# Performance work log

Measured on AMD Instinct MI355X. Metric: run time of the kernel, lower is better.

Reference implementation:

```python
import jax, jax.numpy as jnp
import numpy as np

N_NODES = 100000
N_EDGES = 640000
D_IN = 128
D_OUT = 128
D_HID = 128  # assumed MLP hidden width (repo MLP not shown; standard 2-layer GIN MLP)


def setup_inputs() -> dict:
    key = jax.random.key(0)
    k = jax.random.split(key, 8)
    x = jax.random.normal(k[0], (N_NODES, D_IN), dtype=jnp.float32)
    edge_index = jax.random.randint(k[1], (2, N_EDGES), 0, N_NODES, dtype=jnp.int64)
    edge_attr = jax.random.normal(k[2], (N_EDGES, D_IN), dtype=jnp.float32)
    # learned params
    eps = jnp.zeros((), dtype=jnp.float32)  # train_eps=True, init 0
    s1 = 1.0 / np.sqrt(D_IN)
    s2 = 1.0 / np.sqrt(D_HID)
    W1 = jax.random.uniform(k[3], (D_IN, D_HID), jnp.float32, -s1, s1)
    b1 = jax.random.uniform(k[4], (D_HID,), jnp.float32, -s1, s1)
    W2 = jax.random.uniform(k[5], (D_HID, D_OUT), jnp.float32, -s2, s2)
    b2 = jax.random.uniform(k[6], (D_OUT,), jnp.float32, -s2, s2)
    return {"x": x, "edge_index": edge_index, "edge_attr": edge_attr,
            "eps": eps, "W1": W1, "b1": b1, "W2": W2, "b2": b2}


def reference(x, edge_index, edge_attr, eps, W1, b1, W2, b2):
    src = edge_index[0]  # source nodes j
    dst = edge_index[1]  # target nodes i
    # message: ReLU(x_j + edge_attr)  -- [E, D_IN]
    msg = jax.nn.relu(x[src] + edge_attr)
    # scatter-sum aggregation to target nodes -- [N, D_IN]
    aggr = jax.ops.segment_sum(msg, dst, num_segments=N_NODES)
    # GINE update: (1 + eps) * x_i + aggr, then MLP (dropout=0.0 -> identity)
    h = (1.0 + eps) * x + aggr
    h = jax.nn.relu(h @ W1 + b1)
    out = h @ W2 + b2
    return out
```

## Files before the change

kernel.cpp:

```cpp
#include <hip/hip_runtime.h>
#include <hip/hip_bf16.h>

constexpr int NN = 100000;
constexpr int NE = 640000;
constexpr int D  = 128;
constexpr int NB = (NN + 255) / 256;

typedef __attribute__((ext_vector_type(8))) short bf16x8;
typedef __attribute__((ext_vector_type(4))) float f32x4;

__device__ __forceinline__ short f2bf(float f) {
    union { float f; unsigned u; } v; v.f = f;
    unsigned r = v.u + 0x7FFF + ((v.u >> 16) & 1);
    return (short)(r >> 16);
}
__device__ __forceinline__ float bf2f(short h) {
    union { unsigned u; float f; } v;
    v.u = ((unsigned)(unsigned short)h) << 16;
    return v.f;
}
__device__ __forceinline__ unsigned cvtpk(float a, float b) {
    union { __hip_bfloat162 h2; unsigned u; } cv;
    float2 f; f.x = a; f.y = b;
    cv.h2 = __float22bfloat162_rn(f);
    return cv.u;
}
__device__ __forceinline__ void pack_hilo(const float* v, bf16x8& hi, bf16x8& lo) {
#pragma unroll
    for (int i = 0; i < 4; ++i) {
        unsigned u = cvtpk(v[2 * i], v[2 * i + 1]);
        short h0 = (short)(u & 0xFFFF), h1 = (short)(u >> 16);
        hi[2 * i] = h0; hi[2 * i + 1] = h1;
        unsigned ul = cvtpk(v[2 * i] - bf2f(h0), v[2 * i + 1] - bf2f(h1));
        lo[2 * i] = (short)(ul & 0xFFFF); lo[2 * i + 1] = (short)(ul >> 16);
    }
}
__device__ __forceinline__ bf16x8 pack_bf8(const float* v) {
    bf16x8 o;
#pragma unroll
    for (int i = 0; i < 4; ++i) {
        unsigned u = cvtpk(v[2 * i], v[2 * i + 1]);
        o[2 * i] = (short)(u & 0xFFFF); o[2 * i + 1] = (short)(u >> 16);
    }
    return o;
}

__global__ __launch_bounds__(256) void k_zero(int* __restrict__ cnt) {
    int i = blockIdx.x * 256 + threadIdx.x;
    if (i < NN) cnt[i] = 0;
}

__global__ __launch_bounds__(256) void k_hist(const int* __restrict__ dst,
                                              int* __restrict__ cnt) {
    int e = blockIdx.x * 256 + threadIdx.x;
    if (e < NE) atomicAdd(&cnt[dst[e]], 1);
}

__global__ __launch_bounds__(256) void k_bsum(const int* __restrict__ cnt,
                                              int* __restrict__ bsum) {
    int i = blockIdx.x * 256 + threadIdx.x;
    int v = (i < NN) ? cnt[i] : 0;
#pragma unroll
    for (int s = 32; s; s >>= 1) v += __shfl_down(v, s, 64);
    __shared__ int w[4];
    if ((threadIdx.x & 63) == 0) w[threadIdx.x >> 6] = v;
    __syncthreads();
    if (threadIdx.x == 0) bsum[blockIdx.x] = w[0] + w[1] + w[2] + w[3];
}

__global__ __launch_bounds__(512) void k_scan_bsum(const int* __restrict__ bsum,
                                                   int* __restrict__ bboff) {
    int t = threadIdx.x, lane = t & 63;
    int v = (t < NB) ? bsum[t] : 0;
    int incl = v;
#pragma unroll
    for (int s = 1; s < 64; s <<= 1) {
        int u = __shfl_up(incl, s, 64);
        if (lane >= s) incl += u;
    }
    __shared__ int wt[8], wp[8];
    if (lane == 63) wt[t >> 6] = incl;
    __syncthreads();
    if (t == 0) { int run = 0; for (int i = 0; i < 8; ++i) { wp[i] = run; run += wt[i]; } }
    __syncthreads();
    if (t < NB) bboff[t] = incl - v + wp[t >> 6];
}

__global__ __launch_bounds__(256) void k_scan_final(const int* __restrict__ cnt,
                                                    const int* __restrict__ bboff,
                                                    int* __restrict__ off,
                                                    int* __restrict__ cur) {
    int b = blockIdx.x, t = threadIdx.x, lane = t & 63;
    int i = b * 256 + t;
    int v = (i < NN) ? cnt[i] : 0;
    int incl = v;
#pragma unroll
    for (int s = 1; s < 64; s <<= 1) {
        int u = __shfl_up(incl, s, 64);
        if (lane >= s) incl += u;
    }
    __shared__ int wt[4], wp[4];
    if (lane == 63) wt[t >> 6] = incl;
    __syncthreads();
    if (t == 0) { int run = 0; for (int q = 0; q < 4; ++q) { wp[q] = run; run += wt[q]; } }
    __syncthreads();
    int excl = incl - v + wp[t >> 6] + bboff[b];
    if (i < NN) { off[i] = excl; cur[i] = excl; }
    if (i == 0) off[NN] = NE;
}

__global__ __launch_bounds__(256) void k_perm(const int* __restrict__ dst,
                                              const int* __restrict__ src,
                                              int* __restrict__ cur,
                                              int2* __restrict__ ps) {
    int e = blockIdx.x * 256 + threadIdx.x;
    if (e < NE) {
        int p = atomicAdd(&cur[dst[e]], 1);
        int2 v; v.x = e; v.y = src[e];
        ps[p] = v;
    }
}

__global__ __launch_bounds__(256) void k_wsplit(const float* __restrict__ W,
                                                short* __restrict__ Whi,
                                                short* __restrict__ Wlo) {
    for (int idx = blockIdx.x * 256 + threadIdx.x; idx < D * D; idx += gridDim.x * 256) {
        int n = idx >> 7, k = idx & 127;
        float w = W[k * D + n];
        short hi = f2bf(w);
        Whi[idx] = hi;
        Wlo[idx] = f2bf(w - bf2f(hi));
    }
}

constexpr int LDG = 132;

__global__ __launch_bounds__(256) void k_fused(const float* __restrict__ x,
                                               const float* __restrict__ ea,
                                               const int* __restrict__ off,
                                               const int2* __restrict__ ps,
                                               const float* __restrict__ eps,
                                               const short* __restrict__ W1h,
                                               const short* __restrict__ W1l,
                                               const short* __restrict__ W2h,
                                               const short* __restrict__ W2l,
                                               const float* __restrict__ b1,
                                               const float* __restrict__ b2,
                                               float* __restrict__ out) {
    __shared__ float G1[32 * LDG];
    __shared__ float G2[32 * LDG];

    const int wave = threadIdx.x >> 6;
    const int lane = threadIdx.x & 63;
    const int nb = blockIdx.x * 32;

    {
        const int lo2 = lane * 2;
        const float sc = 1.0f + eps[0];
        for (int t = 0; t < 8; ++t) {
            const int n = nb + wave * 8 + t;
            const int j0 = off[n], j1 = off[n + 1];
            float accx = 0.0f, accy = 0.0f;
            for (int j = j0; j < j1; j += 8) {
                int ee[8], ss[8];
#pragma unroll
                for (int q = 0; q < 8; ++q) {
                    int jj = j + q; jj = (jj < j1) ? jj : (j1 - 1);
                    int2 p = ps[jj];
                    ee[q] = p.x; ss[q] = p.y;
                }
                float2 xa[8], eb[8];
#pragma unroll
                for (int q = 0; q < 8; ++q) {
                    xa[q] = *reinterpret_cast<const float2*>(x  + (size_t)ss[q] * D + lo2);
                    eb[q] = *reinterpret_cast<const float2*>(ea + (size_t)ee[q] * D + lo2);
                }
#pragma unroll
                for (int q = 0; q < 8; ++q) {
                    float mx = fmaxf(xa[q].x + eb[q].x, 0.0f);
                    float my = fmaxf(xa[q].y + eb[q].y, 0.0f);
                    bool ok = (j + q) < j1;
                    accx += ok ? mx : 0.0f;
                    accy += ok ? my : 0.0f;
                }
            }
            float2 xx = *reinterpret_cast<const float2*>(x + (size_t)n * D + lo2);
            float2 o;
            o.x = fmaf(sc, xx.x, accx);
            o.y = fmaf(sc, xx.y, accy);
            *reinterpret_cast<float2*>(&G1[(wave * 8 + t) * LDG + lo2]) = o;
        }
    }
    __syncthreads();

    const int r = lane & 15;
    const int g = lane >> 4;

    {
        f32x4 acc[2][2];
#pragma unroll
        for (int mt = 0; mt < 2; ++mt)
#pragma unroll
            for (int nl = 0; nl < 2; ++nl) {
                acc[mt][nl].x = 0.f; acc[mt][nl].y = 0.f;
                acc[mt][nl].z = 0.f; acc[mt][nl].w = 0.f;
            }

#pragma unroll
        for (int kc = 0; kc < 4; ++kc) {
            const int k0 = kc * 32;
            bf16x8 ahi[2], alo[2];
#pragma unroll
            for (int mt = 0; mt < 2; ++mt) {
                const float* gp = &G1[(mt * 16 + r) * LDG + k0 + g * 8];
                float vals[8];
                *reinterpret_cast<float4*>(&vals[0]) = reinterpret_cast<const float4*>(gp)[0];
                *reinterpret_cast<float4*>(&vals[4]) = reinterpret_cast<const float4*>(gp)[1];
                pack_hilo(vals, ahi[mt], alo[mt]);
            }
#pragma unroll
            for (int nl = 0; nl < 2; ++nl) {
                const int nt = wave * 2 + nl;
                const int wb = (nt * 16 + r) * D + k0 + g * 8;
                bf16x8 whi = *reinterpret_cast<const bf16x8*>(&W1h[wb]);
                bf16x8 wlo = *reinterpret_cast<const bf16x8*>(&W1l[wb]);
#pragma unroll
                for (int mt = 0; mt < 2; ++mt) {
                    acc[mt][nl] = __builtin_amdgcn_mfma_f32_16x16x32_bf16(ahi[mt], whi, acc[mt][nl], 0, 0, 0);
                    acc[mt][nl] = __builtin_amdgcn_mfma_f32_16x16x32_bf16(ahi[mt], wlo, acc[mt][nl], 0, 0, 0);
                    acc[mt][nl] = __builtin_amdgcn_mfma_f32_16x16x32_bf16(alo[mt], whi, acc[mt][nl], 0, 0, 0);
                }
            }
        }

#pragma unroll
        for (int nl = 0; nl < 2; ++nl) {
            const int col = (wave * 2 + nl) * 16 + r;
            const float bb = b1[col];
#pragma unroll
            for (int mt = 0; mt < 2; ++mt)
#pragma unroll
                for (int q = 0; q < 4; ++q)
                    G2[(mt * 16 + g * 4 + q) * LDG + col] = fmaxf(acc[mt][nl][q] + bb, 0.0f);
        }
    }
    __syncthreads();

    {
        f32x4 acc[2][2];
#pragma unroll
        for (int mt = 0; mt < 2; ++mt)
#pragma unroll
            for (int nl = 0; nl < 2; ++nl) {
                acc[mt][nl].x = 0.f; acc[mt][nl].y = 0.f;
                acc[mt][nl].z = 0.f; acc[mt][nl].w = 0.f;
            }

#pragma unroll
        for (int kc = 0; kc < 4; ++kc) {
            const int k0 = kc * 32;
            bf16x8 a[2];
#pragma unroll
            for (int mt = 0; mt < 2; ++mt) {
                const float* gp = &G2[(mt * 16 + r) * LDG + k0 + g * 8];
                float vals[8];
                *reinterpret_cast<float4*>(&vals[0]) = reinterpret_cast<const float4*>(gp)[0];
                *reinterpret_cast<float4*>(&vals[4]) = reinterpret_cast<const float4*>(gp)[1];
                a[mt] = pack_bf8(vals);
            }
#pragma unroll
            for (int nl = 0; nl < 2; ++nl) {
                const int nt = wave * 2 + nl;
                const int wb = (nt * 16 + r) * D + k0 + g * 8;
                bf16x8 whi = *reinterpret_cast<const bf16x8*>(&W2h[wb]);
                bf16x8 wlo = *reinterpret_cast<const bf16x8*>(&W2l[wb]);
#pragma unroll
                for (int mt = 0; mt < 2; ++mt) {
                    acc[mt][nl] = __builtin_amdgcn_mfma_f32_16x16x32_bf16(a[mt], whi, acc[mt][nl], 0, 0, 0);
                    acc[mt][nl] = __builtin_amdgcn_mfma_f32_16x16x32_bf16(a[mt], wlo, acc[mt][nl], 0, 0, 0);
                }
            }
        }

#pragma unroll
        for (int nl = 0; nl < 2; ++nl) {
            const int col = (wave * 2 + nl) * 16 + r;
            const float bb = b2[col];
#pragma unroll
            for (int mt = 0; mt < 2; ++mt)
#pragma unroll
                for (int q = 0; q < 4; ++q) {
                    long row = nb + mt * 16 + g * 4 + q;
                    out[row * D + col] = acc[mt][nl][q] + bb;
                }
        }
    }
}

extern "C" void kernel_launch(void* const* d_in, const int* in_sizes, int n_in,
                              void* d_out, int out_size, void* d_ws, size_t ws_size,
                              hipStream_t stream) {
    const float* x   = (const float*)d_in[0];
    const int*   ei  = (const int*)d_in[1];
    const float* ea  = (const float*)d_in[2];
    const float* eps = (const float*)d_in[3];
    const float* W1  = (const float*)d_in[4];
    const float* b1  = (const float*)d_in[5];
    const float* W2  = (const float*)d_in[6];
    const float* b2  = (const float*)d_in[7];
    float* out = (float*)d_out;

    const int* src = ei;
    const int* dst = ei + NE;

    int* base  = (int*)d_ws;
    int* cnt   = base;
    int* off   = cnt + NN;
    int* cur   = off + NN + 1;
    int* bsum  = cur + NN;
    int* bboff = bsum + NB;
    size_t ps_off = ((size_t)(3 * NN + 1 + 2 * NB) + 1) & ~(size_t)1;
    int2* ps   = (int2*)(base + ps_off);
    short* wsp = (short*)(base + ps_off + 2 * (size_t)NE);
    short* W1h = wsp;
    short* W1l = W1h + D * D;
    short* W2h = W1l + D * D;
    short* W2l = W2h + D * D;

    k_wsplit    <<<32,               256, 0, stream>>>(W1, W1h, W1l);
    k_wsplit    <<<32,               256, 0, stream>>>(W2, W2h, W2l);
    k_zero      <<<NB,               256, 0, stream>>>(cnt);
    k_hist      <<<(NE + 255) / 256, 256, 0, stream>>>(dst, cnt);
    k_bsum      <<<NB,               256, 0, stream>>>(cnt, bsum);
    k_scan_bsum <<<1,                512, 0, stream>>>(bsum, bboff);
    k_scan_final<<<NB,               256, 0, stream>>>(cnt, bboff, off, cur);
    k_perm      <<<(NE + 255) / 256, 256, 0, stream>>>(dst, src, cur, ps);

    k_fused<<<NN / 32, 256, 0, stream>>>(x, ea, off, ps, eps,
                                         W1h, W1l, W2h, W2l, b1, b2, out);
}
```

Before: 265.3 us.

## Bin edges by 32-node blocks and stream bf16 messages into per-bin buffer

Replaces the per-node CSR build (histogram, scans, permutation) with a coarse 32-node bin histogram and a single-block scan. A new message kernel reads edge_attr and x[src] once per edge with coalesced rows, computes ReLU messages, and writes them as bf16 into a bin-ordered buffer. The fused MLP kernel then accumulates each bin's messages into shared memory with LDS atomics before the GEMMs. This avoids scattered edge_attr gathers in the fused kernel and several small launches, but adds a large intermediate write and read of bf16 messages plus the rounding error from storing messages in bf16.

Result: slower. 660.7 us (+149.0%).

```diff
diff --git a/kernel.cpp b/kernel.cpp
--- a/kernel.cpp
+++ b/kernel.cpp
@@ -1,12 +1,17 @@
 #include <hip/hip_runtime.h>
 #include <hip/hip_bf16.h>
 
-constexpr int NN = 100000;
-constexpr int NE = 640000;
-constexpr int D  = 128;
-constexpr int NB = (NN + 255) / 256;
+constexpr int NN  = 100000;
+constexpr int NE  = 640000;
+constexpr int D   = 128;
+constexpr int BIN = 32;
+constexpr int KB2 = NN / BIN;
+constexpr int CPAD = 32;
+constexpr int NHB = 64;
+constexpr int LDG = 132;
 
 typedef __attribute__((ext_vector_type(8))) short bf16x8;
+typedef __attribute__((ext_vector_type(8))) unsigned short u16x8;
 typedef __attribute__((ext_vector_type(4))) float f32x4;
 
 __device__ __forceinline__ short f2bf(float f) {
@@ -43,82 +48,6 @@
         o[2 * i] = (short)(u & 0xFFFF); o[2 * i + 1] = (short)(u >> 16);
     }
     return o;
-}
-
-__global__ __launch_bounds__(256) void k_zero(int* __restrict__ cnt) {
-    int i = blockIdx.x * 256 + threadIdx.x;
-    if (i < NN) cnt[i] = 0;
-}
-
-__global__ __launch_bounds__(256) void k_hist(const int* __restrict__ dst,
-                                              int* __restrict__ cnt) {
-    int e = blockIdx.x * 256 + threadIdx.x;
-    if (e < NE) atomicAdd(&cnt[dst[e]], 1);
-}
-
-__global__ __launch_bounds__(256) void k_bsum(const int* __restrict__ cnt,
-                                              int* __restrict__ bsum) {
-    int i = blockIdx.x * 256 + threadIdx.x;
-    int v = (i < NN) ? cnt[i] : 0;
-#pragma unroll
-    for (int s = 32; s; s >>= 1) v += __shfl_down(v, s, 64);
-    __shared__ int w[4];
-    if ((threadIdx.x & 63) == 0) w[threadIdx.x >> 6] = v;
-    __syncthreads();
-    if (threadIdx.x == 0) bsum[blockIdx.x] = w[0] + w[1] + w[2] + w[3];
-}
-
-__global__ __launch_bounds__(512) void k_scan_bsum(const int* __restrict__ bsum,
-                                                   int* __restrict__ bboff) {
-    int t = threadIdx.x, lane = t & 63;
-    int v = (t < NB) ? bsum[t] : 0;
-    int incl = v;
-#pragma unroll
-    for (int s = 1; s < 64; s <<= 1) {
-        int u = __shfl_up(incl, s, 64);
-        if (lane >= s) incl += u;
-    }
-    __shared__ int wt[8], wp[8];
-    if (lane == 63) wt[t >> 6] = incl;
-    __syncthreads();
-    if (t == 0) { int run = 0; for (int i = 0; i < 8; ++i) { wp[i] = run; run += wt[i]; } }
-    __syncthreads();
-    if (t < NB) bboff[t] = incl - v + wp[t >> 6];
-}
-
-__global__ __launch_bounds__(256) void k_scan_final(const int* __restrict__ cnt,
-                                                    const int* __restrict__ bboff,
-                                                    int* __restrict__ off,
-                                                    int* __restrict__ cur) {
-    int b = blockIdx.x, t = threadIdx.x, lane = t & 63;
-    int i = b * 256 + t;
-    int v = (i < NN) ? cnt[i] : 0;
-    int incl = v;
-#pragma unroll
-    for (int s = 1; s < 64; s <<= 1) {
-        int u = __shfl_up(incl, s, 64);
-        if (lane >= s) incl += u;
-    }
-    __shared__ int wt[4], wp[4];
-    if (lane == 63) wt[t >> 6] = incl;
-    __syncthreads();
-    if (t == 0) { int run = 0; for (int q = 0; q < 4; ++q) { wp[q] = run; run += wt[q]; } }
-    __syncthreads();
-    int excl = incl - v + wp[t >> 6] + bboff[b];
-    if (i < NN) { off[i] = excl; cur[i] = excl; }
-    if (i == 0) off[NN] = NE;
-}
-
-__global__ __launch_bounds__(256) void k_perm(const int* __restrict__ dst,
-                                              const int* __restrict__ src,
-                                              int* __restrict__ cur,
-                                              int2* __restrict__ ps) {
-    int e = blockIdx.x * 256 + threadIdx.x;
-    if (e < NE) {
-        int p = atomicAdd(&cur[dst[e]], 1);
-        int2 v; v.x = e; v.y = src[e];
-        ps[p] = v;
-    }
 }
 
 __global__ __launch_bounds__(256) void k_wsplit(const float* __restrict__ W,
@@ -133,62 +62,130 @@
     }
 }
 
-constexpr int LDG = 132;
-
-__global__ __launch_bounds__(256) void k_fused(const float* __restrict__ x,
-                                               const float* __restrict__ ea,
-                                               const int* __restrict__ off,
-                                               const int2* __restrict__ ps,
-                                               const float* __restrict__ eps,
-                                               const short* __restrict__ W1h,
-                                               const short* __restrict__ W1l,
-                                               const short* __restrict__ W2h,
-                                               const short* __restrict__ W2l,
-                                               const float* __restrict__ b1,
-                                               const float* __restrict__ b2,
-                                               float* __restrict__ out) {
+__global__ __launch_bounds__(256) void k_phist(const int* __restrict__ dst,
+                                               int* __restrict__ part) {
+    __shared__ int lh[KB2];
+    for (int i = threadIdx.x; i < KB2; i += 256) lh[i] = 0;
+    __syncthreads();
+    const int chunk = NE / NHB;
+    const int e0 = blockIdx.x * chunk;
+    for (int e = e0 + threadIdx.x; e < e0 + chunk; e += 256)
+        atomicAdd(&lh[dst[e] >> 5], 1);
+    __syncthreads();
+    int* p = part + blockIdx.x * KB2;
+    for (int i = threadIdx.x; i < KB2; i += 256) p[i] = lh[i];
+}
+
+__global__ __launch_bounds__(1024) void k_bscan(const int* __restrict__ part,
+                                                int* __restrict__ binoff,
+                                                int* __restrict__ cur) {
+    int t = threadIdx.x, lane = t & 63;
+    int c0[4]; int s = 0;
+#pragma unroll
+    for (int q = 0; q < 4; ++q) {
+        int b = t * 4 + q;
+        int v = 0;
+        if (b < KB2)
+            for (int p = 0; p < NHB; ++p) v += part[p * KB2 + b];
+        c0[q] = v; s += v;
+    }
+    int incl = s;
+#pragma unroll
+    for (int sh = 1; sh < 64; sh <<= 1) {
+        int u = __shfl_up(incl, sh, 64);
+        if (lane >= sh) incl += u;
+    }
+    __shared__ int wt[16], wp[16];
+    if (lane == 63) wt[t >> 6] = incl;
+    __syncthreads();
+    if (t == 0) { int run = 0; for (int i = 0; i < 16; ++i) { wp[i] = run; run += wt[i]; } }
+    __syncthreads();
+    int excl = incl - s + wp[t >> 6];
+#pragma unroll
+    for (int q = 0; q < 4; ++q) {
+        int b = t * 4 + q;
+        if (b < KB2) { binoff[b] = excl; cur[b * CPAD] = excl; excl += c0[q]; }
+    }
+    if (t == 0) binoff[KB2] = NE;
+}
+
+__global__ __launch_bounds__(256) void k_msg(const float* __restrict__ x,
+                                             const int* __restrict__ src,
+                                             const int* __restrict__ dst,
+                                             const float* __restrict__ ea,
+                                             int* __restrict__ cur,
+                                             unsigned char* __restrict__ mdst,
+                                             unsigned short* __restrict__ mbuf) {
+    unsigned gid = blockIdx.x * 256 + threadIdx.x;
+    unsigned e = gid >> 4;
+    unsigned c = gid & 15;
+    const int lane = threadIdx.x & 63;
+    const int s = src[e];
+    const int d = dst[e];
+    int slot = 0;
+    if (c == 0) {
+        slot = atomicAdd(&cur[(d >> 5) * CPAD], 1);
+        mdst[slot] = (unsigned char)(d & (BIN - 1));
+    }
+    slot = __shfl(slot, lane & 48, 64);
+
+    const float* xp  = x  + (size_t)s * D + c * 8;
+    const float* eap = ea + (size_t)e * D + c * 8;
+    float4 a0 = reinterpret_cast<const float4*>(xp)[0];
+    float4 a1 = reinterpret_cast<const float4*>(xp)[1];
+    float4 b0 = reinterpret_cast<const float4*>(eap)[0];
+    float4 b1 = reinterpret_cast<const float4*>(eap)[1];
+    float m[8] = {fmaxf(a0.x + b0.x, 0.0f), fmaxf(a0.y + b0.y, 0.0f),
+                  fmaxf(a0.z + b0.z, 0.0f), fmaxf(a0.w + b0.w, 0.0f),
+                  fmaxf(a1.x + b1.x, 0.0f), fmaxf(a1.y + b1.y, 0.0f),
+                  fmaxf(a1.z + b1.z, 0.0f), fmaxf(a1.w + b1.w, 0.0f)};
+    bf16x8 o = pack_bf8(m);
+    *reinterpret_cast<bf16x8*>(mbuf + (size_t)slot * D + c * 8) = o;
+}
+
+__global__ __launch_bounds__(256) void k_fused2(const float* __restrict__ x,
+                                                const unsigned short* __restrict__ mbuf,
+                                                const unsigned char* __restrict__ mdst,
+                                                const int* __restrict__ binoff,
+                                                const float* __restrict__ eps,
+                                                const short* __restrict__ W1h,
+                                                const short* __restrict__ W1l,
+                                                const short* __restrict__ W2h,
+                                                const short* __restrict__ W2l,
+                                                const float* __restrict__ b1,
+                                                const float* __restrict__ b2,
+                                                float* __restrict__ out) {
     __shared__ float G1[32 * LDG];
     __shared__ float G2[32 * LDG];
 
     const int wave = threadIdx.x >> 6;
     const int lane = threadIdx.x & 63;
-    const int nb = blockIdx.x * 32;
+    const int b = blockIdx.x;
+    const int nb = b * BIN;
 
     {
-        const int lo2 = lane * 2;
         const float sc = 1.0f + eps[0];
-        for (int t = 0; t < 8; ++t) {
-            const int n = nb + wave * 8 + t;
-            const int j0 = off[n], j1 = off[n + 1];
-            float accx = 0.0f, accy = 0.0f;
-            for (int j = j0; j < j1; j += 8) {
-                int ee[8], ss[8];
-#pragma unroll
-                for (int q = 0; q < 8; ++q) {
-                    int jj = j + q; jj = (jj < j1) ? jj : (j1 - 1);
-                    int2 p = ps[jj];
-                    ee[q] = p.x; ss[q] = p.y;
-                }
-                float2 xa[8], eb[8];
-#pragma unroll
-                for (int q = 0; q < 8; ++q) {
-                    xa[q] = *reinterpret_cast<const float2*>(x  + (size_t)ss[q] * D + lo2);
-                    eb[q] = *reinterpret_cast<const float2*>(ea + (size_t)ee[q] * D + lo2);
-                }
-#pragma unroll
-                for (int q = 0; q < 8; ++q) {
-                    float mx = fmaxf(xa[q].x + eb[q].x, 0.0f);
-                    float my = fmaxf(xa[q].y + eb[q].y, 0.0f);
-                    bool ok = (j + q) < j1;
-                    accx += ok ? mx : 0.0f;
-                    accy += ok ? my : 0.0f;
-                }
-            }
-            float2 xx = *reinterpret_cast<const float2*>(x + (size_t)n * D + lo2);
-            float2 o;
-            o.x = fmaf(sc, xx.x, accx);
-            o.y = fmaf(sc, xx.y, accy);
-            *reinterpret_cast<float2*>(&G1[(wave * 8 + t) * LDG + lo2]) = o;
+        for (int i = threadIdx.x; i < 32 * 32; i += 256) {
+            int row = i >> 5, q = i & 31;
+            float4 xx = reinterpret_cast<const float4*>(x)[(size_t)(nb + row) * 32 + q];
+            float4 v;
+            v.x = sc * xx.x; v.y = sc * xx.y; v.z = sc * xx.z; v.w = sc * xx.w;
+            *reinterpret_cast<float4*>(&G1[row * LDG + q * 4]) = v;
+        }
+    }
+    __syncthreads();
+
+    {
+        const int j0 = binoff[b], j1 = binoff[b + 1];
+        const int cc = lane & 15;
+        const int half = lane >> 4;
+        for (int m = j0 + wave * 4 + half; m < j1; m += 16) {
+            int ld = mdst[m];
+            u16x8 mv = *reinterpret_cast<const u16x8*>(mbuf + (size_t)m * D + cc * 8);
+            float* ap = &G1[ld * LDG + cc * 8];
+#pragma unroll
+            for (int i = 0; i < 8; ++i)
+                atomicAdd(ap + i, bf2f((short)mv[i]));
         }
     }
     __syncthreads();
@@ -313,29 +310,25 @@
     const int* src = ei;
     const int* dst = ei + NE;
 
-    int* base  = (int*)d_ws;
-    int* cnt   = base;
-    int* off   = cnt + NN;
-    int* cur   = off + NN + 1;
-    int* bsum  = cur + NN;
-    int* bboff = bsum + NB;
-    size_t ps_off = ((size_t)(3 * NN + 1 + 2 * NB) + 1) & ~(size_t)1;
-    int2* ps   = (int2*)(base + ps_off);
-    short* wsp = (short*)(base + ps_off + 2 * (size_t)NE);
+    int* part   = (int*)d_ws;
+    int* binoff = part + NHB * KB2;
+    int* cur    = binoff + KB2 + 1;
+    unsigned char* mdst = (unsigned char*)(cur + KB2 * CPAD);
+    size_t hdr_bytes = (size_t)(NHB * KB2 + KB2 + 1 + KB2 * CPAD) * 4 + NE;
+    size_t mb_off = (hdr_bytes + 255) & ~(size_t)255;
+    unsigned short* mbuf = (unsigned short*)((char*)d_ws + mb_off);
+    short* wsp = (short*)(mbuf + (size_t)NE * D);
     short* W1h = wsp;
     short* W1l = W1h + D * D;
     short* W2h = W1l + D * D;
     short* W2l = W2h + D * D;
 
-    k_wsplit    <<<32,               256, 0, stream>>>(W1, W1h, W1l);
-    k_wsplit    <<<32,               256, 0, stream>>>(W2, W2h, W2l);
-    k_zero      <<<NB,               256, 0, stream>>>(cnt);
-    k_hist      <<<(NE + 255) / 256, 256, 0, stream>>>(dst, cnt);
-    k_bsum      <<<NB,               256, 0, stream>>>(cnt, bsum);
-    k_scan_bsum <<<1,                512, 0, stream>>>(bsum, bboff);
-    k_scan_final<<<NB,               256, 0, stream>>>(cnt, bboff, off, cur);
-    k_perm      <<<(NE + 255) / 256, 256, 0, stream>>>(dst, src, cur, ps);
-
-    k_fused<<<NN / 32, 256, 0, stream>>>(x, ea, off, ps, eps,
-                                         W1h, W1l, W2h, W2l, b1, b2, out);
-}
+    k_wsplit<<<32,  256, 0, stream>>>(W1, W1h, W1l);
+    k_wsplit<<<32,  256, 0, stream>>>(W2, W2h, W2l);
+    k_phist <<<NHB, 256, 0, stream>>>(dst, part);
+    k_bscan <<<1,  1024, 0, stream>>>(part, binoff, cur);
+
+    k_msg<<<NE * 16 / 256, 256, 0, stream>>>(x, src, dst, ea, cur, mdst, mbuf);
+    k_fused2<<<KB2, 256, 0, stream>>>(x, mbuf, mdst, binoff, eps,
+                                      W1h, W1l, W2h, W2l, b1, b2, out);
+}
```
